# Performance work log

Measured on AMD Instinct MI355X. Metric: run time of the kernel, lower is better.

The kernel has to match this reference:

```python
import jax, jax.numpy as jnp
import numpy as np

A, B, M, H, E, N = 1, 32, 32, 1024, 8, 1024

def setup_inputs() -> dict:
    key = jax.random.key(0)
    k1, k2, k3 = jax.random.split(key, 3)
    hidden_4d = jax.random.normal(k1, (A, B, M, H), dtype=jnp.float32)
    sparsity = jax.random.uniform(k2, (A, B, 1, E), dtype=jnp.float32)
    weight = jax.random.normal(k3, (1, E, H, N), dtype=jnp.float32) * 0.02
    return {"hidden_4d": hidden_4d, "sparsity": sparsity, "weight": weight}

def reference(hidden_4d, sparsity, weight):
    # Original: out = einsum('abmh,ehn->abemn'); out *= mask[a,b,e,1,1]; out.sum((-2,-1))
    # The mask is constant over (m, n), so the sum fuses into the contraction:
    # contracted[a,b,e] = sum_{m,h,n} hidden[a,b,m,h] * weight[e,h,n]
    contracted = jnp.einsum('abmh,ehn->abe', hidden_4d, weight[0])  # (A,B,E)
    mask = jnp.squeeze(sparsity, axis=2)  # (A,B,E)
    return contracted * mask
```

## Files before the change

kernel.cpp:

```cpp
#include <hip/hip_runtime.h>


#define Bdim 32
#define Mdim 32
#define Hdim 1024
#define Edim 8
#define Ndim 1024

__global__ __launch_bounds__(256) void reduce_kernel(
    const float* __restrict__ hidden,
    const float* __restrict__ weight,
    float* __restrict__ ws)
{
    constexpr int NB_W = 512;
    if (blockIdx.x < NB_W) {
        const int wave = blockIdx.x * 4 + (threadIdx.x >> 6);
        const int lane = threadIdx.x & 63;
        const float4* w4 = reinterpret_cast<const float4*>(weight);
        #pragma unroll
        for (int r = 0; r < 4; ++r) {
            const int row = wave * 4 + r;
            float s = 0.f;
            #pragma unroll
            for (int j = 0; j < 4; ++j) {
                float4 v = w4[row * (Ndim / 4) + j * 64 + lane];
                s += (v.x + v.y) + (v.z + v.w);
            }
            #pragma unroll
            for (int off = 32; off > 0; off >>= 1)
                s += __shfl_xor(s, off, 64);
            if (lane == 0) ws[row] = s;
        }
    } else {
        const int idx = (blockIdx.x - NB_W) * 256 + threadIdx.x;
        const int b = idx >> 10;
        const int h = idx & 1023;
        const float* p = hidden + b * (Mdim * Hdim) + h;
        float s = 0.f;
        #pragma unroll
        for (int m = 0; m < Mdim; ++m) s += p[m * Hdim];
        ws[Edim * Hdim + idx] = s;
    }
}

__global__ __launch_bounds__(256) void dot_kernel(
    const float* __restrict__ ws,
    const float* __restrict__ sparsity,
    float* __restrict__ out)
{
    const int o = blockIdx.x * 4 + (threadIdx.x >> 6);
    const int lane = threadIdx.x & 63;
    const int b = o >> 3;
    const int e = o & 7;
    const float* hsum = ws + Edim * Hdim + b * Hdim;
    const float* wsum = ws + e * Hdim;
    float s = 0.f;
    #pragma unroll
    for (int j = 0; j < 16; ++j) {
        const int h = j * 64 + lane;
        s += hsum[h] * wsum[h];
    }
    #pragma unroll
    for (int off = 32; off > 0; off >>= 1)
        s += __shfl_xor(s, off, 64);
    if (lane == 0) out[o] = s * sparsity[o];
}

extern "C" void kernel_launch(void* const* d_in, const int* in_sizes, int n_in,
                              void* d_out, int out_size, void* d_ws, size_t ws_size,
                              hipStream_t stream) {
    const float* hidden   = (const float*)d_in[0];
    const float* sparsity = (const float*)d_in[1];
    const float* weight   = (const float*)d_in[2];
    float* out = (float*)d_out;
    float* ws  = (float*)d_ws;

    reduce_kernel<<<640, 256, 0, stream>>>(hidden, weight, ws);
    dot_kernel<<<64, 256, 0, stream>>>(ws, sparsity, out);
}
```

Baseline: 79.40 us.

## Fuse weight and hidden reductions with dot product via per-chunk atomics

Merges the two-kernel reduce-then-dot pipeline into one kernel. Each block takes an (expert, 16-row H chunk), reduces the weight rows and the hidden M-sums for that chunk into shared memory, forms partial dots for all 32 batches, and atomically adds them into the output, which is zeroed by a memset. This removes the workspace round trip and the second kernel launch. In exchange, every block recomputes the hidden sums for its chunk, so hidden is read 8 times, once per expert, and the result now depends on atomics and a memset.

Result: slower. 93.28 us (+17.5%).

```diff
diff --git a/kernel.cpp b/kernel.cpp
--- a/kernel.cpp
+++ b/kernel.cpp
@@ -6,20 +6,28 @@
 #define Hdim 1024
 #define Edim 8
 #define Ndim 1024
+#define CHUNK 16
 
-__global__ __launch_bounds__(256) void reduce_kernel(
+__global__ __launch_bounds__(256) void fused_kernel(
     const float* __restrict__ hidden,
     const float* __restrict__ weight,
-    float* __restrict__ ws)
+    const float* __restrict__ sparsity,
+    float* __restrict__ out)
 {
-    constexpr int NB_W = 512;
-    if (blockIdx.x < NB_W) {
-        const int wave = blockIdx.x * 4 + (threadIdx.x >> 6);
+    __shared__ float wsum_l[CHUNK];
+    __shared__ float hsum_l[Bdim][CHUNK + 1];
+
+    const int e  = blockIdx.x >> 6;
+    const int hc = blockIdx.x & 63;
+    const int h0 = hc * CHUNK;
+
+    {
+        const int wave = threadIdx.x >> 6;
         const int lane = threadIdx.x & 63;
         const float4* w4 = reinterpret_cast<const float4*>(weight);
         #pragma unroll
         for (int r = 0; r < 4; ++r) {
-            const int row = wave * 4 + r;
+            const int row = e * Hdim + h0 + wave * 4 + r;
             float s = 0.f;
             #pragma unroll
             for (int j = 0; j < 4; ++j) {
@@ -29,41 +37,35 @@
             #pragma unroll
             for (int off = 32; off > 0; off >>= 1)
                 s += __shfl_xor(s, off, 64);
-            if (lane == 0) ws[row] = s;
+            if (lane == 0) wsum_l[wave * 4 + r] = s;
         }
-    } else {
-        const int idx = (blockIdx.x - NB_W) * 256 + threadIdx.x;
-        const int b = idx >> 10;
-        const int h = idx & 1023;
-        const float* p = hidden + b * (Mdim * Hdim) + h;
+    }
+
+    {
+        const int hp = threadIdx.x & 15;
+        const int q  = threadIdx.x >> 4;
+        #pragma unroll
+        for (int b2 = 0; b2 < 2; ++b2) {
+            const int b = q + 16 * b2;
+            const float* p = hidden + b * (Mdim * Hdim) + h0 + hp;
+            float s = 0.f;
+            #pragma unroll
+            for (int m = 0; m < Mdim; ++m) s += p[m * Hdim];
+            hsum_l[b][hp] = s;
+        }
+    }
+
+    __syncthreads();
+
+    if (threadIdx.x < Bdim) {
+        const int b = threadIdx.x;
         float s = 0.f;
         #pragma unroll
-        for (int m = 0; m < Mdim; ++m) s += p[m * Hdim];
-        ws[Edim * Hdim + idx] = s;
+        for (int h = 0; h < CHUNK; ++h)
+            s += hsum_l[b][h] * wsum_l[h];
+        const int o = b * Edim + e;
+        atomicAdd(&out[o], s * sparsity[o]);
     }
-}
-
-__global__ __launch_bounds__(256) void dot_kernel(
-    const float* __restrict__ ws,
-    const float* __restrict__ sparsity,
-    float* __restrict__ out)
-{
-    const int o = blockIdx.x * 4 + (threadIdx.x >> 6);
-    const int lane = threadIdx.x & 63;
-    const int b = o >> 3;
-    const int e = o & 7;
-    const float* hsum = ws + Edim * Hdim + b * Hdim;
-    const float* wsum = ws + e * Hdim;
-    float s = 0.f;
-    #pragma unroll
-    for (int j = 0; j < 16; ++j) {
-        const int h = j * 64 + lane;
-        s += hsum[h] * wsum[h];
-    }
-    #pragma unroll
-    for (int off = 32; off > 0; off >>= 1)
-        s += __shfl_xor(s, off, 64);
-    if (lane == 0) out[o] = s * sparsity[o];
 }
 
 extern "C" void kernel_launch(void* const* d_in, const int* in_sizes, int n_in,
@@ -73,8 +75,7 @@
     const float* sparsity = (const float*)d_in[1];
     const float* weight   = (const float*)d_in[2];
     float* out = (float*)d_out;
-    float* ws  = (float*)d_ws;
 
-    reduce_kernel<<<640, 256, 0, stream>>>(hidden, weight, ws);
-    dot_kernel<<<64, 256, 0, stream>>>(ws, sparsity, out);
+    hipMemsetAsync(out, 0, Bdim * Edim * sizeof(float), stream);
+    fused_kernel<<<Edim * (Hdim / CHUNK), 256, 0, stream>>>(hidden, weight, sparsity, out);
 }
```
